# Kernel optimization log

Measured on AMD Instinct MI355X. Metric: run time of the kernel, lower is better.

Reference implementation:

```python
import jax, jax.numpy as jnp
import numpy as np

B, S, D, H, HD, F = 8, 1024, 512, 8, 64, 2048
EPS = 1e-6

def rmsnorm(x, w):
    var = jnp.mean(x * x, axis=-1, keepdims=True)
    return w * (x * jax.lax.rsqrt(var + EPS))

def setup_inputs() -> dict:
    key = jax.random.key(0)
    ks = jax.random.split(key, 10)
    sd = 512 ** -0.5
    return {
        "primals_1": jax.random.normal(ks[0], (D, D), jnp.float32) * sd,
        "primals_2": jax.random.normal(ks[1], (D, D), jnp.float32) * sd,
        "primals_3": jax.random.normal(ks[2], (D, D), jnp.float32) * sd,
        "primals_4": jax.random.normal(ks[3], (D, D), jnp.float32) * sd,
        "primals_5": jax.random.uniform(ks[4], (D,), jnp.float32, 0.5, 1.5),
        "primals_6": jax.random.normal(ks[5], (F, D), jnp.float32) * sd,
        "primals_7": jax.random.normal(ks[6], (D, F), jnp.float32) * (F ** -0.5),
        "primals_8": jax.random.uniform(ks[7], (D,), jnp.float32, 0.5, 1.5),
        "primals_9": jax.random.normal(ks[8], (B, S, D), jnp.float32),
        "primals_10": jax.random.normal(ks[9], (B, H, S, S), jnp.float32) * 0.1,
    }

def reference(primals_1, primals_2, primals_3, primals_4, primals_5,
              primals_6, primals_7, primals_8, primals_9, primals_10):
    x = primals_9
    # --- self-attention sublayer ---
    h = rmsnorm(x, primals_5)                      # [B,S,D]
    # T5: no 1/sqrt(head_dim) scaling
    q = (h @ primals_3.T).reshape(B, S, H, HD).transpose(0, 2, 1, 3)  # [B,H,S,HD]
    k = (h @ primals_1.T).reshape(B, S, H, HD).transpose(0, 2, 1, 3)
    v = (h @ primals_4.T).reshape(B, S, H, HD).transpose(0, 2, 1, 3)
    scores = jnp.einsum('bhqd,bhkd->bhqk', q, k) + primals_10        # [B,H,S,S]
    attn = jax.nn.softmax(scores, axis=-1)
    ctx = jnp.einsum('bhqk,bhkd->bhqd', attn, v)                     # [B,H,S,HD]
    ctx = ctx.transpose(0, 2, 1, 3).reshape(B, S, D)
    x = x + ctx @ primals_2.T                       # residual add_1
    # --- FFN sublayer ---
    h2 = rmsnorm(x, primals_8)
    ff = jax.nn.relu(h2 @ primals_6.T)              # [B,S,F]
    out = x + ff @ primals_7.T                      # add_3
    return out
```

## Files before the change

### kernel.cpp

```cpp
#include <hip/hip_runtime.h>

#define B_ 8
#define S_ 1024
#define D_ 512
#define H_ 8
#define HD_ 64
#define F_ 2048

typedef unsigned short u16;
typedef __attribute__((ext_vector_type(8))) short bf16x8;
typedef __attribute__((ext_vector_type(4))) float f32x4;

__device__ __forceinline__ float bf2f(u16 u) {
  union { unsigned int i; float f; } v; v.i = ((unsigned int)u) << 16; return v.f;
}
__device__ __forceinline__ u16 f2bf(float f) {
  union { float f; unsigned int i; } v; v.f = f;
  unsigned int r = v.i + 0x7fffu + ((v.i >> 16) & 1u);
  return (u16)(r >> 16);
}

__device__ __forceinline__ void gl2lds16(const u16* g, u16* lds) {
  __builtin_amdgcn_global_load_lds(
      (const __attribute__((address_space(1))) unsigned int*)g,
      (__attribute__((address_space(3))) unsigned int*)lds, 16, 0, 0);
}

__global__ __launch_bounds__(256) void cvt_w_k(const float* __restrict__ w0, const float* __restrict__ w1,
                                               const float* __restrict__ w2, const float* __restrict__ w3,
                                               const float* __restrict__ w4, const float* __restrict__ w5,
                                               u16* __restrict__ dst) {
  size_t gid = (size_t)blockIdx.x * 256 + threadIdx.x;
  size_t e0 = gid * 4;
  const float* src; size_t loc;
  if      (e0 <  262144) { src = w0; loc = e0; }
  else if (e0 <  524288) { src = w1; loc = e0 -  262144; }
  else if (e0 <  786432) { src = w2; loc = e0 -  524288; }
  else if (e0 < 1048576) { src = w3; loc = e0 -  786432; }
  else if (e0 < 2097152) { src = w4; loc = e0 - 1048576; }
  else                   { src = w5; loc = e0 - 2097152; }
  float4 v = *(const float4*)(src + loc);
  ushort4 o; o.x = f2bf(v.x); o.y = f2bf(v.y); o.z = f2bf(v.z); o.w = f2bf(v.w);
  *(ushort4*)(dst + e0) = o;
}

template <int IN_BF16>
__global__ __launch_bounds__(256) void rmsnorm_k(const void* __restrict__ xv,
                                                 const float* __restrict__ w,
                                                 u16* __restrict__ out) {
  int row = blockIdx.x;
  int tid = threadIdx.x;
  float x0, x1;
  if (IN_BF16) {
    const u16* xr = (const u16*)xv + (size_t)row * D_;
    x0 = bf2f(xr[tid]); x1 = bf2f(xr[tid + 256]);
  } else {
    const float* xr = (const float*)xv + (size_t)row * D_;
    x0 = xr[tid]; x1 = xr[tid + 256];
  }
  float s = x0 * x0 + x1 * x1;
#pragma unroll
  for (int off = 32; off >= 1; off >>= 1) s += __shfl_xor(s, off, 64);
  __shared__ float red[4];
  int lane = tid & 63, wid = tid >> 6;
  if (lane == 0) red[wid] = s;
  __syncthreads();
  float tot = red[0] + red[1] + red[2] + red[3];
  float inv = rsqrtf(tot * (1.0f / D_) + 1e-6f);
  u16* orow = out + (size_t)row * D_;
  orow[tid]       = f2bf(x0 * inv * w[tid]);
  orow[tid + 256] = f2bf(x1 * inv * w[tid + 256]);
}

template <int RELU, int RMODE, int OF32>
__global__ __launch_bounds__(256) void gemm_mfma_k(const u16* __restrict__ A,
                                                   const u16* __restrict__ W,
                                                   const void* __restrict__ Rv,
                                                   void* __restrict__ Cv,
                                                   int M, int N, int K) {
  __shared__ __align__(16) u16 As[128 * 32];
  __shared__ __align__(16) u16 Bs[128 * 32];
  int tid = threadIdx.x;
  int w = tid >> 6, l = tid & 63;
  int quad = l >> 4, l16 = l & 15;
  int m0 = blockIdx.y * 128, n0 = blockIdx.x * 128;
  int wr = (w >> 1) * 64, wc = (w & 1) * 64;

  int c_sw = (l & 3) ^ ((l >> 2) & 3);
  int r_in = l >> 2;
  int swz = quad ^ (l16 & 3);

  f32x4 acc[4][4];
#pragma unroll
  for (int i = 0; i < 4; i++)
#pragma unroll
    for (int j = 0; j < 4; j++) acc[i][j] = (f32x4)(0.0f);

  for (int k0 = 0; k0 < K; k0 += 32) {
    __syncthreads();
#pragma unroll
    for (int t = 0; t < 2; t++) {
      int chunk = w * 2 + t;
      int row = chunk * 16 + r_in;
      gl2lds16(A + (size_t)(m0 + row) * K + k0 + c_sw * 8, As + chunk * 512);
      gl2lds16(W + (size_t)(n0 + row) * K + k0 + c_sw * 8, Bs + chunk * 512);
    }
    __syncthreads();
    bf16x8 af[4], bf[4];
#pragma unroll
    for (int i = 0; i < 4; i++)
      af[i] = *(const bf16x8*)(As + (wr + i * 16 + l16) * 32 + swz * 8);
#pragma unroll
    for (int j = 0; j < 4; j++)
      bf[j] = *(const bf16x8*)(Bs + (wc + j * 16 + l16) * 32 + swz * 8);
#pragma unroll
    for (int i = 0; i < 4; i++)
#pragma unroll
      for (int j = 0; j < 4; j++)
        acc[i][j] = __builtin_amdgcn_mfma_f32_16x16x32_bf16(af[i], bf[j], acc[i][j], 0, 0, 0);
  }

#pragma unroll
  for (int i = 0; i < 4; i++)
#pragma unroll
    for (int r = 0; r < 4; r++) {
      int mrow = m0 + wr + i * 16 + quad * 4 + r;
      size_t base = (size_t)mrow * N + n0 + wc + l16;
#pragma unroll
      for (int j = 0; j < 4; j++) {
        float v = acc[i][j][r];
        if (RELU) v = fmaxf(v, 0.0f);
        if (RMODE == 1) v += ((const float*)Rv)[base + j * 16];
        if (RMODE == 2) v += bf2f(((const u16*)Rv)[base + j * 16]);
        if (OF32) ((float*)Cv)[base + j * 16] = v;
        else      ((u16*)Cv)[base + j * 16]   = f2bf(v);
      }
    }
}

__global__ __launch_bounds__(256) void attn_mfma_k(const u16* __restrict__ Q,
                                                   const u16* __restrict__ K,
                                                   const u16* __restrict__ V,
                                                   const float* __restrict__ bias,
                                                   u16* __restrict__ ctx) {
  int tid = threadIdx.x;
  int w = tid >> 6, lane = tid & 63;
  int quad = lane >> 4, l16 = lane & 15;
  int h = blockIdx.y, b = blockIdx.z;
  int q0 = blockIdx.x * 64;

  __shared__ __align__(16) u16 Ks[32][72];
  __shared__ __align__(16) u16 Vt[64][40];
  __shared__ __align__(16) u16 Pl[4][16][40];

  size_t qbase = ((size_t)(b * S_) + q0 + w * 16 + l16) * D_ + h * HD_;
  bf16x8 qf0 = *(const bf16x8*)(Q + qbase + quad * 8);
  bf16x8 qf1 = *(const bf16x8*)(Q + qbase + 32 + quad * 8);

  float mr[4], lr[4];
  f32x4 Oacc[4];
#pragma unroll
  for (int r = 0; r < 4; r++) { mr[r] = -1e30f; lr[r] = 0.0f; }
#pragma unroll
  for (int nt = 0; nt < 4; nt++) Oacc[nt] = (f32x4)(0.0f);

  const float* bp = bias + (((size_t)(b * H_ + h) * S_) + q0 + w * 16) * S_;

  int skey = tid >> 3;
  int sd8  = (tid & 7) * 8;

  for (int kt = 0; kt < S_; kt += 32) {
    __syncthreads();
    size_t kb = ((size_t)(b * S_) + kt + skey) * D_ + h * HD_ + sd8;
    bf16x8 kv = *(const bf16x8*)(K + kb);
    *(bf16x8*)(&Ks[skey][sd8]) = kv;
    bf16x8 vv = *(const bf16x8*)(V + kb);
#pragma unroll
    for (int i = 0; i < 8; i++) Vt[sd8 + i][skey] = (u16)((short*)&vv)[i];
    __syncthreads();

    f32x4 s1 = (f32x4)(0.0f), s2 = (f32x4)(0.0f);
    {
      bf16x8 kf;
      kf = *(const bf16x8*)(&Ks[l16][quad * 8]);
      s1 = __builtin_amdgcn_mfma_f32_16x16x32_bf16(qf0, kf, s1, 0, 0, 0);
      kf = *(const bf16x8*)(&Ks[l16][32 + quad * 8]);
      s1 = __builtin_amdgcn_mfma_f32_16x16x32_bf16(qf1, kf, s1, 0, 0, 0);
      kf = *(const bf16x8*)(&Ks[16 + l16][quad * 8]);
      s2 = __builtin_amdgcn_mfma_f32_16x16x32_bf16(qf0, kf, s2, 0, 0, 0);
      kf = *(const bf16x8*)(&Ks[16 + l16][32 + quad * 8]);
      s2 = __builtin_amdgcn_mfma_f32_16x16x32_bf16(qf1, kf, s2, 0, 0, 0);
    }
#pragma unroll
    for (int r = 0; r < 4; r++) {
      const float* bpr = bp + (size_t)(quad * 4 + r) * S_ + kt;
      s1[r] += bpr[l16];
      s2[r] += bpr[16 + l16];
    }
#pragma unroll
    for (int r = 0; r < 4; r++) {
      float t = fmaxf(s1[r], s2[r]);
      t = fmaxf(t, __shfl_xor(t, 1, 64));
      t = fmaxf(t, __shfl_xor(t, 2, 64));
      t = fmaxf(t, __shfl_xor(t, 4, 64));
      t = fmaxf(t, __shfl_xor(t, 8, 64));
      float mn = fmaxf(mr[r], t);
      float alpha = __expf(mr[r] - mn);
      float p1 = __expf(s1[r] - mn);
      float p2 = __expf(s2[r] - mn);
      float rs = p1 + p2;
      rs += __shfl_xor(rs, 1, 64);
      rs += __shfl_xor(rs, 2, 64);
      rs += __shfl_xor(rs, 4, 64);
      rs += __shfl_xor(rs, 8, 64);
      lr[r] = lr[r] * alpha + rs;
      mr[r] = mn;
#pragma unroll
      for (int nt = 0; nt < 4; nt++) Oacc[nt][r] *= alpha;
      Pl[w][quad * 4 + r][l16]      = f2bf(p1);
      Pl[w][quad * 4 + r][16 + l16] = f2bf(p2);
    }
    bf16x8 pf = *(const bf16x8*)(&Pl[w][l16][quad * 8]);
#pragma unroll
    for (int nt = 0; nt < 4; nt++) {
      bf16x8 vf = *(const bf16x8*)(&Vt[nt * 16 + l16][quad * 8]);
      Oacc[nt] = __builtin_amdgcn_mfma_f32_16x16x32_bf16(pf, vf, Oacc[nt], 0, 0, 0);
    }
  }

  size_t obase = ((size_t)(b * S_) + q0 + w * 16) * D_ + h * HD_;
#pragma unroll
  for (int r = 0; r < 4; r++) {
    float inv = 1.0f / lr[r];
    int qr = quad * 4 + r;
#pragma unroll
    for (int nt = 0; nt < 4; nt++) {
      ctx[obase + (size_t)qr * D_ + nt * 16 + l16] = f2bf(Oacc[nt][r] * inv);
    }
  }
}

extern "C" void kernel_launch(void* const* d_in, const int* in_sizes, int n_in,
                              void* d_out, int out_size, void* d_ws, size_t ws_size,
                              hipStream_t stream) {
  const float* Wk   = (const float*)d_in[0];
  const float* Wo   = (const float*)d_in[1];
  const float* Wq   = (const float*)d_in[2];
  const float* Wv   = (const float*)d_in[3];
  const float* g1   = (const float*)d_in[4];
  const float* Wf1  = (const float*)d_in[5];
  const float* Wf2  = (const float*)d_in[6];
  const float* g2   = (const float*)d_in[7];
  const float* X    = (const float*)d_in[8];
  const float* bias = (const float*)d_in[9];
  float* out = (float*)d_out;

  const size_t MD = (size_t)B_ * S_ * D_;
  const size_t WB = 3145728;
  u16* wbf  = (u16*)d_ws;
  u16* Wkb  = wbf;
  u16* Wob  = wbf +  262144;
  u16* Wqb  = wbf +  524288;
  u16* Wvb  = wbf +  786432;
  u16* Wf1b = wbf + 1048576;
  u16* Wf2b = wbf + 2097152;
  u16* slot = wbf + WB;
  u16* h    = slot;
  u16* q    = slot + MD;
  u16* k    = slot + 2 * MD;
  u16* v    = slot + 3 * MD;
  u16* ctx  = slot + 4 * MD;
  u16* x1   = h;
  u16* h2   = q;
  u16* ff   = k;

  dim3 blk(256);
  const int M = B_ * S_;

  cvt_w_k<<<3072, blk, 0, stream>>>(Wk, Wo, Wq, Wv, Wf1, Wf2, wbf);

  rmsnorm_k<0><<<M, blk, 0, stream>>>(X, g1, h);

  dim3 g512(D_ / 128, M / 128);
  gemm_mfma_k<0, 0, 0><<<g512, blk, 0, stream>>>(h, Wqb, nullptr, q, M, D_, D_);
  gemm_mfma_k<0, 0, 0><<<g512, blk, 0, stream>>>(h, Wkb, nullptr, k, M, D_, D_);
  gemm_mfma_k<0, 0, 0><<<g512, blk, 0, stream>>>(h, Wvb, nullptr, v, M, D_, D_);

  dim3 ga(S_ / 64, H_, B_);
  attn_mfma_k<<<ga, blk, 0, stream>>>(q, k, v, bias, ctx);

  gemm_mfma_k<0, 1, 0><<<g512, blk, 0, stream>>>(ctx, Wob, X, x1, M, D_, D_);

  rmsnorm_k<1><<<M, blk, 0, stream>>>(x1, g2, h2);

  dim3 gff1(F_ / 128, M / 128);
  gemm_mfma_k<1, 0, 0><<<gff1, blk, 0, stream>>>(h2, Wf1b, nullptr, ff, M, F_, D_);

  gemm_mfma_k<0, 2, 1><<<g512, blk, 0, stream>>>(ff, Wf2b, x1, out, M, D_, F_);
}
```

Measured before the change: 605.2 us.

## Fuse QKV projections into one GEMM and pre-transpose V for attention

Reorders the weight conversion so Wq, Wk and Wv sit contiguously, then replaces three projection GEMMs with a single N=1536 GEMM writing an interleaved QKV buffer. A separate kernel transposes V per head so the attention kernel can stream K and V^T straight into swizzled LDS with global_load_lds, with no scalar LDS transpose inside the loop. The attention loop also moves from 32 to 64 keys per iteration, which halves the number of barriers and softmax rescale steps. The cost is an extra kernel launch, an extra pass over V through memory, and a larger workspace.

Result: faster. 580.3 us (-4.1%).

```diff
diff --git a/kernel.cpp b/kernel.cpp
--- a/kernel.cpp
+++ b/kernel.cpp
@@ -26,19 +26,19 @@
       (__attribute__((address_space(3))) unsigned int*)lds, 16, 0, 0);
 }
 
-__global__ __launch_bounds__(256) void cvt_w_k(const float* __restrict__ w0, const float* __restrict__ w1,
-                                               const float* __restrict__ w2, const float* __restrict__ w3,
-                                               const float* __restrict__ w4, const float* __restrict__ w5,
+__global__ __launch_bounds__(256) void cvt_w_k(const float* __restrict__ wq, const float* __restrict__ wk,
+                                               const float* __restrict__ wv, const float* __restrict__ wo,
+                                               const float* __restrict__ wf1, const float* __restrict__ wf2,
                                                u16* __restrict__ dst) {
   size_t gid = (size_t)blockIdx.x * 256 + threadIdx.x;
   size_t e0 = gid * 4;
   const float* src; size_t loc;
-  if      (e0 <  262144) { src = w0; loc = e0; }
-  else if (e0 <  524288) { src = w1; loc = e0 -  262144; }
-  else if (e0 <  786432) { src = w2; loc = e0 -  524288; }
-  else if (e0 < 1048576) { src = w3; loc = e0 -  786432; }
-  else if (e0 < 2097152) { src = w4; loc = e0 - 1048576; }
-  else                   { src = w5; loc = e0 - 2097152; }
+  if      (e0 <  262144) { src = wq;  loc = e0; }
+  else if (e0 <  524288) { src = wk;  loc = e0 -  262144; }
+  else if (e0 <  786432) { src = wv;  loc = e0 -  524288; }
+  else if (e0 < 1048576) { src = wo;  loc = e0 -  786432; }
+  else if (e0 < 2097152) { src = wf1; loc = e0 - 1048576; }
+  else                   { src = wf2; loc = e0 - 2097152; }
   float4 v = *(const float4*)(src + loc);
   ushort4 o; o.x = f2bf(v.x); o.y = f2bf(v.y); o.z = f2bf(v.z); o.w = f2bf(v.w);
   *(ushort4*)(dst + e0) = o;
@@ -138,24 +138,47 @@
     }
 }
 
-__global__ __launch_bounds__(256) void attn_mfma_k(const u16* __restrict__ Q,
-                                                   const u16* __restrict__ K,
-                                                   const u16* __restrict__ V,
-                                                   const float* __restrict__ bias,
-                                                   u16* __restrict__ ctx) {
+__global__ __launch_bounds__(256) void transpose_v_k(const u16* __restrict__ qkv,
+                                                     u16* __restrict__ vt) {
+  __shared__ u16 T[64][72];
+  int t = threadIdx.x;
+  int s0 = blockIdx.x * 64, h = blockIdx.y, b = blockIdx.z;
+  int skey = t >> 3, dch = (t & 7) * 8;
+#pragma unroll
+  for (int rnd = 0; rnd < 2; rnd++) {
+    int s = s0 + skey + rnd * 32;
+    bf16x8 vv = *(const bf16x8*)(qkv + ((size_t)(b * S_) + s) * 1536 + 1024 + h * HD_ + dch);
+#pragma unroll
+    for (int i = 0; i < 8; i++) T[dch + i][skey + rnd * 32] = (u16)((short*)&vv)[i];
+  }
+  __syncthreads();
+  int d = t >> 2, kc = (t & 3) * 16;
+  bf16x8 a0 = *(const bf16x8*)(&T[d][kc]);
+  bf16x8 a1 = *(const bf16x8*)(&T[d][kc + 8]);
+  u16* dst = vt + ((size_t)(b * H_ + h) * HD_ + d) * S_ + s0 + kc;
+  *(bf16x8*)dst       = a0;
+  *(bf16x8*)(dst + 8) = a1;
+}
+
+__global__ __launch_bounds__(256) void attn_v2_k(const u16* __restrict__ qkv,
+                                                 const u16* __restrict__ vt,
+                                                 const float* __restrict__ bias,
+                                                 u16* __restrict__ ctx) {
   int tid = threadIdx.x;
   int w = tid >> 6, lane = tid & 63;
   int quad = lane >> 4, l16 = lane & 15;
   int h = blockIdx.y, b = blockIdx.z;
   int q0 = blockIdx.x * 64;
 
-  __shared__ __align__(16) u16 Ks[32][72];
-  __shared__ __align__(16) u16 Vt[64][40];
-  __shared__ __align__(16) u16 Pl[4][16][40];
-
-  size_t qbase = ((size_t)(b * S_) + q0 + w * 16 + l16) * D_ + h * HD_;
-  bf16x8 qf0 = *(const bf16x8*)(Q + qbase + quad * 8);
-  bf16x8 qf1 = *(const bf16x8*)(Q + qbase + 32 + quad * 8);
+  __shared__ __align__(16) u16 KsA[64 * 32];
+  __shared__ __align__(16) u16 KsB[64 * 32];
+  __shared__ __align__(16) u16 VsA[64 * 32];
+  __shared__ __align__(16) u16 VsB[64 * 32];
+  __shared__ __align__(16) u16 Pl[4][16 * 72];
+
+  const u16* qrow = qkv + ((size_t)(b * S_) + q0 + w * 16 + l16) * 1536 + h * HD_;
+  bf16x8 qf0 = *(const bf16x8*)(qrow + quad * 8);
+  bf16x8 qf1 = *(const bf16x8*)(qrow + 32 + quad * 8);
 
   float mr[4], lr[4];
   f32x4 Oacc[4];
@@ -164,51 +187,58 @@
 #pragma unroll
   for (int nt = 0; nt < 4; nt++) Oacc[nt] = (f32x4)(0.0f);
 
-  const float* bp = bias + (((size_t)(b * H_ + h) * S_) + q0 + w * 16) * S_;
-
-  int skey = tid >> 3;
-  int sd8  = (tid & 7) * 8;
-
-  for (int kt = 0; kt < S_; kt += 32) {
+  const float* bpw = bias + ((size_t)((b * H_ + h) * S_) + q0 + w * 16) * S_;
+
+  int srow = w * 16 + (lane >> 2);
+  int sc   = lane & 3;
+  int slc  = sc ^ (srow & 3);
+  u16* ldsKA = KsA + w * 512;
+  u16* ldsKB = KsB + w * 512;
+  u16* ldsVA = VsA + w * 512;
+  u16* ldsVB = VsB + w * 512;
+
+  for (int kt = 0; kt < S_; kt += 64) {
     __syncthreads();
-    size_t kb = ((size_t)(b * S_) + kt + skey) * D_ + h * HD_ + sd8;
-    bf16x8 kv = *(const bf16x8*)(K + kb);
-    *(bf16x8*)(&Ks[skey][sd8]) = kv;
-    bf16x8 vv = *(const bf16x8*)(V + kb);
-#pragma unroll
-    for (int i = 0; i < 8; i++) Vt[sd8 + i][skey] = (u16)((short*)&vv)[i];
+    {
+      const u16* krow = qkv + ((size_t)(b * S_) + kt + srow) * 1536 + 512 + h * HD_;
+      gl2lds16(krow + slc * 8, ldsKA);
+      gl2lds16(krow + 32 + slc * 8, ldsKB);
+      const u16* vrow = vt + ((size_t)(b * H_ + h) * HD_ + srow) * S_ + kt;
+      gl2lds16(vrow + slc * 8, ldsVA);
+      gl2lds16(vrow + 32 + slc * 8, ldsVB);
+    }
     __syncthreads();
 
-    f32x4 s1 = (f32x4)(0.0f), s2 = (f32x4)(0.0f);
-    {
-      bf16x8 kf;
-      kf = *(const bf16x8*)(&Ks[l16][quad * 8]);
-      s1 = __builtin_amdgcn_mfma_f32_16x16x32_bf16(qf0, kf, s1, 0, 0, 0);
-      kf = *(const bf16x8*)(&Ks[l16][32 + quad * 8]);
-      s1 = __builtin_amdgcn_mfma_f32_16x16x32_bf16(qf1, kf, s1, 0, 0, 0);
-      kf = *(const bf16x8*)(&Ks[16 + l16][quad * 8]);
-      s2 = __builtin_amdgcn_mfma_f32_16x16x32_bf16(qf0, kf, s2, 0, 0, 0);
-      kf = *(const bf16x8*)(&Ks[16 + l16][32 + quad * 8]);
-      s2 = __builtin_amdgcn_mfma_f32_16x16x32_bf16(qf1, kf, s2, 0, 0, 0);
+    f32x4 sg[4];
+#pragma unroll
+    for (int g = 0; g < 4; g++) {
+      int row = g * 16 + l16;
+      int sw = quad ^ (row & 3);
+      bf16x8 kf0 = *(const bf16x8*)(KsA + row * 32 + sw * 8);
+      bf16x8 kf1 = *(const bf16x8*)(KsB + row * 32 + sw * 8);
+      f32x4 a = (f32x4)(0.0f);
+      a = __builtin_amdgcn_mfma_f32_16x16x32_bf16(qf0, kf0, a, 0, 0, 0);
+      a = __builtin_amdgcn_mfma_f32_16x16x32_bf16(qf1, kf1, a, 0, 0, 0);
+      sg[g] = a;
     }
 #pragma unroll
     for (int r = 0; r < 4; r++) {
-      const float* bpr = bp + (size_t)(quad * 4 + r) * S_ + kt;
-      s1[r] += bpr[l16];
-      s2[r] += bpr[16 + l16];
-    }
-#pragma unroll
-    for (int r = 0; r < 4; r++) {
-      float t = fmaxf(s1[r], s2[r]);
+      size_t bro = (size_t)(quad * 4 + r) * S_ + kt + l16;
+      float b0 = bpw[bro];
+      float b1 = bpw[bro + 16];
+      float b2 = bpw[bro + 32];
+      float b3 = bpw[bro + 48];
+      float s0 = sg[0][r] + b0, s1 = sg[1][r] + b1, s2 = sg[2][r] + b2, s3 = sg[3][r] + b3;
+      float t = fmaxf(fmaxf(s0, s1), fmaxf(s2, s3));
       t = fmaxf(t, __shfl_xor(t, 1, 64));
       t = fmaxf(t, __shfl_xor(t, 2, 64));
       t = fmaxf(t, __shfl_xor(t, 4, 64));
       t = fmaxf(t, __shfl_xor(t, 8, 64));
       float mn = fmaxf(mr[r], t);
       float alpha = __expf(mr[r] - mn);
-      float p1 = __expf(s1[r] - mn);
-      float p2 = __expf(s2[r] - mn);
-      float rs = p1 + p2;
+      float p0 = __expf(s0 - mn), p1 = __expf(s1 - mn);
+      float p2 = __expf(s2 - mn), p3 = __expf(s3 - mn);
+      float rs = (p0 + p1) + (p2 + p3);
       rs += __shfl_xor(rs, 1, 64);
       rs += __shfl_xor(rs, 2, 64);
       rs += __shfl_xor(rs, 4, 64);
@@ -217,14 +247,22 @@
       mr[r] = mn;
 #pragma unroll
       for (int nt = 0; nt < 4; nt++) Oacc[nt][r] *= alpha;
-      Pl[w][quad * 4 + r][l16]      = f2bf(p1);
-      Pl[w][quad * 4 + r][16 + l16] = f2bf(p2);
-    }
-    bf16x8 pf = *(const bf16x8*)(&Pl[w][l16][quad * 8]);
+      u16* prow = &Pl[w][(quad * 4 + r) * 72];
+      prow[l16]      = f2bf(p0);
+      prow[16 + l16] = f2bf(p1);
+      prow[32 + l16] = f2bf(p2);
+      prow[48 + l16] = f2bf(p3);
+    }
+    bf16x8 pf0 = *(const bf16x8*)(&Pl[w][l16 * 72 + quad * 8]);
+    bf16x8 pf1 = *(const bf16x8*)(&Pl[w][l16 * 72 + 32 + quad * 8]);
 #pragma unroll
     for (int nt = 0; nt < 4; nt++) {
-      bf16x8 vf = *(const bf16x8*)(&Vt[nt * 16 + l16][quad * 8]);
-      Oacc[nt] = __builtin_amdgcn_mfma_f32_16x16x32_bf16(pf, vf, Oacc[nt], 0, 0, 0);
+      int row = nt * 16 + l16;
+      int sw = quad ^ (row & 3);
+      bf16x8 vf0 = *(const bf16x8*)(VsA + row * 32 + sw * 8);
+      bf16x8 vf1 = *(const bf16x8*)(VsB + row * 32 + sw * 8);
+      Oacc[nt] = __builtin_amdgcn_mfma_f32_16x16x32_bf16(pf0, vf0, Oacc[nt], 0, 0, 0);
+      Oacc[nt] = __builtin_amdgcn_mfma_f32_16x16x32_bf16(pf1, vf1, Oacc[nt], 0, 0, 0);
     }
   }
 
@@ -256,39 +294,36 @@
   float* out = (float*)d_out;
 
   const size_t MD = (size_t)B_ * S_ * D_;
-  const size_t WB = 3145728;
-  u16* wbf  = (u16*)d_ws;
-  u16* Wkb  = wbf;
-  u16* Wob  = wbf +  262144;
-  u16* Wqb  = wbf +  524288;
-  u16* Wvb  = wbf +  786432;
-  u16* Wf1b = wbf + 1048576;
-  u16* Wf2b = wbf + 2097152;
-  u16* slot = wbf + WB;
-  u16* h    = slot;
-  u16* q    = slot + MD;
-  u16* k    = slot + 2 * MD;
-  u16* v    = slot + 3 * MD;
-  u16* ctx  = slot + 4 * MD;
-  u16* x1   = h;
-  u16* h2   = q;
-  u16* ff   = k;
+  u16* wbf   = (u16*)d_ws;
+  u16* Wqkvb = wbf;
+  u16* Wob   = wbf +  786432;
+  u16* Wf1b  = wbf + 1048576;
+  u16* Wf2b  = wbf + 2097152;
+  u16* h     = wbf + 3145728;
+  u16* qkv   = h + MD;
+  u16* vtb   = qkv + 3 * MD;
+  u16* ctx   = vtb + MD;
+  u16* ff    = ctx + MD;
+  u16* x1    = qkv;
+  u16* h2    = h;
 
   dim3 blk(256);
   const int M = B_ * S_;
 
-  cvt_w_k<<<3072, blk, 0, stream>>>(Wk, Wo, Wq, Wv, Wf1, Wf2, wbf);
+  cvt_w_k<<<3072, blk, 0, stream>>>(Wq, Wk, Wv, Wo, Wf1, Wf2, wbf);
 
   rmsnorm_k<0><<<M, blk, 0, stream>>>(X, g1, h);
 
+  dim3 gqkv(1536 / 128, M / 128);
+  gemm_mfma_k<0, 0, 0><<<gqkv, blk, 0, stream>>>(h, Wqkvb, nullptr, qkv, M, 1536, D_);
+
+  dim3 gt(S_ / 64, H_, B_);
+  transpose_v_k<<<gt, blk, 0, stream>>>(qkv, vtb);
+
+  dim3 ga(S_ / 64, H_, B_);
+  attn_v2_k<<<ga, blk, 0, stream>>>(qkv, vtb, bias, ctx);
+
   dim3 g512(D_ / 128, M / 128);
-  gemm_mfma_k<0, 0, 0><<<g512, blk, 0, stream>>>(h, Wqb, nullptr, q, M, D_, D_);
-  gemm_mfma_k<0, 0, 0><<<g512, blk, 0, stream>>>(h, Wkb, nullptr, k, M, D_, D_);
-  gemm_mfma_k<0, 0, 0><<<g512, blk, 0, stream>>>(h, Wvb, nullptr, v, M, D_, D_);
-
-  dim3 ga(S_ / 64, H_, B_);
-  attn_mfma_k<<<ga, blk, 0, stream>>>(q, k, v, bias, ctx);
-
   gemm_mfma_k<0, 1, 0><<<g512, blk, 0, stream>>>(ctx, Wob, X, x1, M, D_, D_);
 
   rmsnorm_k<1><<<M, blk, 0, stream>>>(x1, g2, h2);
```
